# Kernel tuning notes

Measured on AMD Instinct MI355X. Metric: run time of the kernel, lower is better.

## Reference

```python
import jax, jax.numpy as jnp
import numpy as np

B = 512       # batch/feature rows
N = 131072    # node dimension (last axis of x)
E = 131072    # edges per tree level
L = 4         # number of tree levels


def setup_inputs() -> dict:
    key = jax.random.key(0)
    kx, k0, k1, k2, k3 = jax.random.split(key, 5)
    x = jax.random.normal(kx, (B, N), dtype=jnp.float32)
    edges0 = jax.random.randint(k0, (2, E), 0, N, dtype=jnp.int64)
    edges1 = jax.random.randint(k1, (2, E), 0, N, dtype=jnp.int64)
    edges2 = jax.random.randint(k2, (2, E), 0, N, dtype=jnp.int64)
    edges3 = jax.random.randint(k3, (2, E), 0, N, dtype=jnp.int64)
    return {"x": x, "edges0": edges0, "edges1": edges1,
            "edges2": edges2, "edges3": edges3}


def reference(x, edges0, edges1, edges2, edges3):
    # TreeAggregation.forward: iterate levels from deepest (last) to root
    # (first). Per level: gather x at src along last dim, scatter-add into
    # dst (duplicate dst indices accumulate, matching torch.index_add).
    for edges in (edges3, edges2, edges1, edges0):
        src = edges[0, :]
        dst = edges[1, :]
        values = x[:, src]                 # [B, E] gather
        x = x.at[:, dst].add(values)       # scatter-add with duplicates
    return x
```

## Files before the change

### kernel.cpp

```cpp
#include <hip/hip_runtime.h>
#include <hip/hip_bf16.h>

#define BATCH 512
#define NNODE 131072
#define NEDGE 131072
#define NLAYER 4
#define SCAN_BLK 1024
#define SCAN_NBLK (NNODE / SCAN_BLK)
#define PCAP (8 * NEDGE)

__device__ int g_counts[NLAYER][NNODE];
__device__ int g_offs[NLAYER][NNODE];
__device__ int g_cursor[NLAYER][NNODE];
__device__ int g_srcl[NLAYER][NEDGE];
__device__ int g_bsums[NLAYER][SCAN_NBLK];

__device__ int p_cnt[2][NNODE];
__device__ int p_offs[2][NNODE];
__device__ int p_srcl[2][PCAP];
__device__ int p_bsums[2][SCAN_NBLK];

typedef unsigned int uivec4 __attribute__((ext_vector_type(4)));
typedef float fvec4 __attribute__((ext_vector_type(4)));

__device__ __forceinline__ void nt_store_u4(uint4* p, uint4 v) {
    uivec4 w = {v.x, v.y, v.z, v.w};
    __builtin_nontemporal_store(w, reinterpret_cast<uivec4*>(p));
}

__device__ __forceinline__ void nt_store_f4(float* p, float4 v) {
    fvec4 w = {v.x, v.y, v.z, v.w};
    __builtin_nontemporal_store(w, reinterpret_cast<fvec4*>(p));
}

__global__ void zero_counts_k() {
    int i = blockIdx.x * blockDim.x + threadIdx.x;
    ((int*)g_counts)[i] = 0;
}

__global__ void hist_k(const int* __restrict__ p0, const int* __restrict__ p1,
                       const int* __restrict__ p2, const int* __restrict__ p3) {
    int i = blockIdx.x * blockDim.x + threadIdx.x;
    int layer = i >> 17;
    int e = i & (NEDGE - 1);
    const int* eg = layer == 0 ? p0 : layer == 1 ? p1 : layer == 2 ? p2 : p3;
    atomicAdd(&g_counts[layer][eg[NEDGE + e]], 1);
}

__global__ void scan_block_k() {
    __shared__ int sh[SCAN_BLK];
    int layer = blockIdx.x / SCAN_NBLK;
    int blk = blockIdx.x % SCAN_NBLK;
    int t = threadIdx.x;
    int i = blk * SCAN_BLK + t;
    int own = g_counts[layer][i];
    sh[t] = own;
    __syncthreads();
    for (int off = 1; off < SCAN_BLK; off <<= 1) {
        int v = (t >= off) ? sh[t - off] : 0;
        __syncthreads();
        sh[t] += v;
        __syncthreads();
    }
    g_offs[layer][i] = sh[t] - own;
    if (t == SCAN_BLK - 1) g_bsums[layer][blk] = sh[t];
}

__global__ void scan_bsums_k() {
    __shared__ int sh[SCAN_NBLK];
    int layer = blockIdx.x;
    int t = threadIdx.x;
    int own = g_bsums[layer][t];
    sh[t] = own;
    __syncthreads();
    for (int off = 1; off < SCAN_NBLK; off <<= 1) {
        int v = (t >= off) ? sh[t - off] : 0;
        __syncthreads();
        sh[t] += v;
        __syncthreads();
    }
    g_bsums[layer][t] = sh[t] - own;
}

__global__ void scan_add_k() {
    int layer = blockIdx.x / SCAN_NBLK;
    int blk = blockIdx.x % SCAN_NBLK;
    int i = blk * SCAN_BLK + threadIdx.x;
    int o = g_offs[layer][i] + g_bsums[layer][blk];
    g_offs[layer][i] = o;
    g_cursor[layer][i] = o;
}

__global__ void fill_k(const int* __restrict__ p0, const int* __restrict__ p1,
                       const int* __restrict__ p2, const int* __restrict__ p3) {
    int i = blockIdx.x * blockDim.x + threadIdx.x;
    int layer = i >> 17;
    int e = i & (NEDGE - 1);
    const int* eg = layer == 0 ? p0 : layer == 1 ? p1 : layer == 2 ? p2 : p3;
    int s = eg[e];
    int d = eg[NEDGE + e];
    int p = atomicAdd(&g_cursor[layer][d], 1);
    g_srcl[layer][p] = s;
}

__global__ void count_pair_k() {
    int i = blockIdx.x * blockDim.x + threadIdx.x;
    int pr = i >> 17;
    int d = i & (NNODE - 1);
    int U = pr * 2, V = pr * 2 + 1;
    int c = 1 + g_counts[U][d];
    int vb = g_offs[V][d], vd = g_counts[V][d];
    for (int j = 0; j < vd; ++j) {
        int s = g_srcl[V][vb + j];
        c += 1 + g_counts[U][s];
    }
    p_cnt[pr][d] = c;
}

__global__ void pscan_block_k() {
    __shared__ int sh[SCAN_BLK];
    int pr = blockIdx.x / SCAN_NBLK;
    int blk = blockIdx.x % SCAN_NBLK;
    int t = threadIdx.x;
    int i = blk * SCAN_BLK + t;
    int own = p_cnt[pr][i];
    sh[t] = own;
    __syncthreads();
    for (int off = 1; off < SCAN_BLK; off <<= 1) {
        int v = (t >= off) ? sh[t - off] : 0;
        __syncthreads();
        sh[t] += v;
        __syncthreads();
    }
    p_offs[pr][i] = sh[t] - own;
    if (t == SCAN_BLK - 1) p_bsums[pr][blk] = sh[t];
}

__global__ void pscan_bsums_k() {
    __shared__ int sh[SCAN_NBLK];
    int pr = blockIdx.x;
    int t = threadIdx.x;
    int own = p_bsums[pr][t];
    sh[t] = own;
    __syncthreads();
    for (int off = 1; off < SCAN_NBLK; off <<= 1) {
        int v = (t >= off) ? sh[t - off] : 0;
        __syncthreads();
        sh[t] += v;
        __syncthreads();
    }
    p_bsums[pr][t] = sh[t] - own;
}

__global__ void pscan_add_k() {
    int pr = blockIdx.x / SCAN_NBLK;
    int blk = blockIdx.x % SCAN_NBLK;
    int i = blk * SCAN_BLK + threadIdx.x;
    p_offs[pr][i] += p_bsums[pr][blk];
}

__global__ void fill_pair_k() {
    int i = blockIdx.x * blockDim.x + threadIdx.x;
    int pr = i >> 17;
    int d = i & (NNODE - 1);
    int U = pr * 2, V = pr * 2 + 1;
    int p = p_offs[pr][d];
    int* buf = p_srcl[pr];
    buf[p++] = d;
    int ub = g_offs[U][d], ud = g_counts[U][d];
    for (int j = 0; j < ud; ++j) buf[p++] = g_srcl[U][ub + j];
    int vb = g_offs[V][d], vd = g_counts[V][d];
    for (int j = 0; j < vd; ++j) {
        int s = g_srcl[V][vb + j];
        buf[p++] = s;
        int sb = g_offs[U][s], sd = g_counts[U][s];
        for (int k = 0; k < sd; ++k) buf[p++] = g_srcl[U][sb + k];
    }
}

__global__ void transpose_bf_k(const float* __restrict__ in, unsigned short* __restrict__ out) {
    __shared__ float tile[64][65];
    int c0 = blockIdx.x * 64;
    int r0 = blockIdx.y * 64;
    int tx = threadIdx.x;
    int ty = threadIdx.y;
    float4 v[4];
#pragma unroll
    for (int i = 0; i < 4; ++i)
        v[i] = *reinterpret_cast<const float4*>(&in[(size_t)(r0 + ty + 16 * i) * NNODE + c0 + 4 * tx]);
#pragma unroll
    for (int i = 0; i < 4; ++i) {
        tile[ty + 16 * i][4 * tx + 0] = v[i].x;
        tile[ty + 16 * i][4 * tx + 1] = v[i].y;
        tile[ty + 16 * i][4 * tx + 2] = v[i].z;
        tile[ty + 16 * i][4 * tx + 3] = v[i].w;
    }
    __syncthreads();
#pragma unroll
    for (int i = 0; i < 4; ++i) {
        int n = c0 + ty + 16 * i;
        ushort4 w;
        __hip_bfloat16 h0 = __float2bfloat16(tile[4 * tx + 0][ty + 16 * i]);
        __hip_bfloat16 h1 = __float2bfloat16(tile[4 * tx + 1][ty + 16 * i]);
        __hip_bfloat16 h2 = __float2bfloat16(tile[4 * tx + 2][ty + 16 * i]);
        __hip_bfloat16 h3 = __float2bfloat16(tile[4 * tx + 3][ty + 16 * i]);
        w.x = *reinterpret_cast<unsigned short*>(&h0);
        w.y = *reinterpret_cast<unsigned short*>(&h1);
        w.z = *reinterpret_cast<unsigned short*>(&h2);
        w.w = *reinterpret_cast<unsigned short*>(&h3);
        *reinterpret_cast<ushort4*>(&out[(size_t)n * BATCH + r0 + 4 * tx]) = w;
    }
}

__device__ __forceinline__ void gacc8(float* a, uint4 v) {
    a[0] += __uint_as_float(v.x << 16);
    a[1] += __uint_as_float(v.x & 0xffff0000u);
    a[2] += __uint_as_float(v.y << 16);
    a[3] += __uint_as_float(v.y & 0xffff0000u);
    a[4] += __uint_as_float(v.z << 16);
    a[5] += __uint_as_float(v.z & 0xffff0000u);
    a[6] += __uint_as_float(v.w << 16);
    a[7] += __uint_as_float(v.w & 0xffff0000u);
}

__device__ __forceinline__ unsigned pack2(float lo, float hi) {
    __hip_bfloat16 l = __float2bfloat16(lo);
    __hip_bfloat16 h = __float2bfloat16(hi);
    return (unsigned)*reinterpret_cast<unsigned short*>(&l) |
           ((unsigned)*reinterpret_cast<unsigned short*>(&h) << 16);
}

__device__ __forceinline__ void gather_body_bf(const uint4* __restrict__ cur,
                                               const int* __restrict__ sl, int deg, int q,
                                               float acc[8]) {
    float A[8] = {0, 0, 0, 0, 0, 0, 0, 0};
    float B_[8] = {0, 0, 0, 0, 0, 0, 0, 0};
    float C_[8] = {0, 0, 0, 0, 0, 0, 0, 0};
    float D_[8] = {0, 0, 0, 0, 0, 0, 0, 0};
    int j = 0;
    for (; j + 4 <= deg; j += 4) {
        uint4 v0 = cur[(size_t)sl[j + 0] * 64 + q];
        uint4 v1 = cur[(size_t)sl[j + 1] * 64 + q];
        uint4 v2 = cur[(size_t)sl[j + 2] * 64 + q];
        uint4 v3 = cur[(size_t)sl[j + 3] * 64 + q];
        gacc8(A, v0);
        gacc8(B_, v1);
        gacc8(C_, v2);
        gacc8(D_, v3);
    }
    for (; j < deg; ++j) {
        uint4 v = cur[(size_t)sl[j] * 64 + q];
        gacc8(A, v);
    }
#pragma unroll
    for (int k = 0; k < 8; ++k) acc[k] = A[k] + B_[k] + C_[k] + D_[k];
}

__global__ void gather_p_k(const uint4* __restrict__ cur, uint4* __restrict__ out,
                           int pr) {
    int t = threadIdx.x;
    int n = blockIdx.x * 8 + (t >> 6);
    int q = t & 63;
    int beg = p_offs[pr][n];
    int deg = p_cnt[pr][n];
    float acc[8];
    gather_body_bf(cur, &p_srcl[pr][beg], deg, q, acc);
    uint4 w;
    w.x = pack2(acc[0], acc[1]);
    w.y = pack2(acc[2], acc[3]);
    w.z = pack2(acc[4], acc[5]);
    w.w = pack2(acc[6], acc[7]);
    nt_store_u4(&out[(size_t)n * 64 + q], w);
}

__global__ void __launch_bounds__(1024) gather_tr_p_k(const uint4* __restrict__ cur,
                                                      float* __restrict__ out, int pr) {
    __shared__ float lds[16][520];
    int t = threadIdx.x;
    int n0 = blockIdx.x * 16;
    int nn = t >> 6;
    int q = t & 63;
    int n = n0 + nn;
    int beg = p_offs[pr][n];
    int deg = p_cnt[pr][n];
    float acc[8];
    gather_body_bf(cur, &p_srcl[pr][beg], deg, q, acc);
    float4* lrow = reinterpret_cast<float4*>(&lds[nn][8 * q]);
    lrow[0] = make_float4(acc[0], acc[1], acc[2], acc[3]);
    lrow[1] = make_float4(acc[4], acc[5], acc[6], acc[7]);
    __syncthreads();
    int c = t & 3;
    int rb = t >> 2;
#pragma unroll
    for (int iter = 0; iter < 2; ++iter) {
        int b = iter * 256 + rb;
        float4 w;
        w.x = lds[4 * c + 0][b];
        w.y = lds[4 * c + 1][b];
        w.z = lds[4 * c + 2][b];
        w.w = lds[4 * c + 3][b];
        nt_store_f4(&out[(size_t)b * NNODE + n0 + 4 * c], w);
    }
}

extern "C" void kernel_launch(void* const* d_in, const int* in_sizes, int n_in,
                              void* d_out, int out_size, void* d_ws, size_t ws_size,
                              hipStream_t stream) {
    const float* x = (const float*)d_in[0];
    const int* p0 = (const int*)d_in[4];
    const int* p1 = (const int*)d_in[3];
    const int* p2 = (const int*)d_in[2];
    const int* p3 = (const int*)d_in[1];

    unsigned short* WS0 = (unsigned short*)d_ws;
    unsigned short* WS1 = WS0 + (size_t)NNODE * BATCH;
    float* OUT = (float*)d_out;

    zero_counts_k<<<NLAYER * NNODE / 1024, 1024, 0, stream>>>();
    hist_k<<<NLAYER * NEDGE / 1024, 1024, 0, stream>>>(p0, p1, p2, p3);
    scan_block_k<<<NLAYER * SCAN_NBLK, SCAN_BLK, 0, stream>>>();
    scan_bsums_k<<<NLAYER, SCAN_NBLK, 0, stream>>>();
    scan_add_k<<<NLAYER * SCAN_NBLK, SCAN_BLK, 0, stream>>>();
    fill_k<<<NLAYER * NEDGE / 1024, 1024, 0, stream>>>(p0, p1, p2, p3);

    count_pair_k<<<2 * NNODE / 1024, 1024, 0, stream>>>();
    pscan_block_k<<<2 * SCAN_NBLK, SCAN_BLK, 0, stream>>>();
    pscan_bsums_k<<<2, SCAN_NBLK, 0, stream>>>();
    pscan_add_k<<<2 * SCAN_NBLK, SCAN_BLK, 0, stream>>>();
    fill_pair_k<<<2 * NNODE / 256, 256, 0, stream>>>();

    transpose_bf_k<<<dim3(NNODE / 64, BATCH / 64), dim3(16, 16), 0, stream>>>(x, WS0);

    gather_p_k<<<NNODE / 8, 512, 0, stream>>>((const uint4*)WS0, (uint4*)WS1, 0);
    gather_tr_p_k<<<NNODE / 16, 1024, 0, stream>>>((const uint4*)WS1, OUT, 1);
}
```

Measured before the change: 506.1 us.

## Split batch dimension into two halves for gather kernels to improve cache locality

```diff
diff --git a/kernel.cpp b/kernel.cpp
--- a/kernel.cpp
+++ b/kernel.cpp
@@ -20,12 +20,12 @@
 __device__ int p_srcl[2][PCAP];
 __device__ int p_bsums[2][SCAN_NBLK];
 
-typedef unsigned int uivec4 __attribute__((ext_vector_type(4)));
+typedef unsigned int uivec2 __attribute__((ext_vector_type(2)));
 typedef float fvec4 __attribute__((ext_vector_type(4)));
 
-__device__ __forceinline__ void nt_store_u4(uint4* p, uint4 v) {
-    uivec4 w = {v.x, v.y, v.z, v.w};
-    __builtin_nontemporal_store(w, reinterpret_cast<uivec4*>(p));
+__device__ __forceinline__ void nt_store_u2(uint2* p, uint2 v) {
+    uivec2 w = {v.x, v.y};
+    __builtin_nontemporal_store(w, reinterpret_cast<uivec2*>(p));
 }
 
 __device__ __forceinline__ void nt_store_f4(float* p, float4 v) {
@@ -212,15 +212,11 @@
     }
 }
 
-__device__ __forceinline__ void gacc8(float* a, uint4 v) {
+__device__ __forceinline__ void gacc4(float* a, uint2 v) {
     a[0] += __uint_as_float(v.x << 16);
     a[1] += __uint_as_float(v.x & 0xffff0000u);
     a[2] += __uint_as_float(v.y << 16);
     a[3] += __uint_as_float(v.y & 0xffff0000u);
-    a[4] += __uint_as_float(v.z << 16);
-    a[5] += __uint_as_float(v.z & 0xffff0000u);
-    a[6] += __uint_as_float(v.w << 16);
-    a[7] += __uint_as_float(v.w & 0xffff0000u);
 }
 
 __device__ __forceinline__ unsigned pack2(float lo, float hi) {
@@ -230,77 +226,73 @@
            ((unsigned)*reinterpret_cast<unsigned short*>(&h) << 16);
 }
 
-__device__ __forceinline__ void gather_body_bf(const uint4* __restrict__ cur,
-                                               const int* __restrict__ sl, int deg, int q,
-                                               float acc[8]) {
-    float A[8] = {0, 0, 0, 0, 0, 0, 0, 0};
-    float B_[8] = {0, 0, 0, 0, 0, 0, 0, 0};
-    float C_[8] = {0, 0, 0, 0, 0, 0, 0, 0};
-    float D_[8] = {0, 0, 0, 0, 0, 0, 0, 0};
+__device__ __forceinline__ void gather_body_bf2(const uint2* __restrict__ cur,
+                                                const int* __restrict__ sl, int deg, int idx,
+                                                float acc[4]) {
+    float A[4] = {0, 0, 0, 0};
+    float B_[4] = {0, 0, 0, 0};
+    float C_[4] = {0, 0, 0, 0};
+    float D_[4] = {0, 0, 0, 0};
     int j = 0;
     for (; j + 4 <= deg; j += 4) {
-        uint4 v0 = cur[(size_t)sl[j + 0] * 64 + q];
-        uint4 v1 = cur[(size_t)sl[j + 1] * 64 + q];
-        uint4 v2 = cur[(size_t)sl[j + 2] * 64 + q];
-        uint4 v3 = cur[(size_t)sl[j + 3] * 64 + q];
-        gacc8(A, v0);
-        gacc8(B_, v1);
-        gacc8(C_, v2);
-        gacc8(D_, v3);
+        uint2 v0 = cur[(size_t)sl[j + 0] * 128 + idx];
+        uint2 v1 = cur[(size_t)sl[j + 1] * 128 + idx];
+        uint2 v2 = cur[(size_t)sl[j + 2] * 128 + idx];
+        uint2 v3 = cur[(size_t)sl[j + 3] * 128 + idx];
+        gacc4(A, v0);
+        gacc4(B_, v1);
+        gacc4(C_, v2);
+        gacc4(D_, v3);
     }
     for (; j < deg; ++j) {
-        uint4 v = cur[(size_t)sl[j] * 64 + q];
-        gacc8(A, v);
+        uint2 v = cur[(size_t)sl[j] * 128 + idx];
+        gacc4(A, v);
     }
 #pragma unroll
-    for (int k = 0; k < 8; ++k) acc[k] = A[k] + B_[k] + C_[k] + D_[k];
-}
-
-__global__ void gather_p_k(const uint4* __restrict__ cur, uint4* __restrict__ out,
-                           int pr) {
+    for (int k = 0; k < 4; ++k) acc[k] = A[k] + B_[k] + C_[k] + D_[k];
+}
+
+__global__ void gather_p_k(const uint2* __restrict__ cur, uint2* __restrict__ out,
+                           int pr, int h) {
     int t = threadIdx.x;
     int n = blockIdx.x * 8 + (t >> 6);
     int q = t & 63;
+    int idx = h * 64 + q;
     int beg = p_offs[pr][n];
     int deg = p_cnt[pr][n];
-    float acc[8];
-    gather_body_bf(cur, &p_srcl[pr][beg], deg, q, acc);
-    uint4 w;
+    float acc[4];
+    gather_body_bf2(cur, &p_srcl[pr][beg], deg, idx, acc);
+    uint2 w;
     w.x = pack2(acc[0], acc[1]);
     w.y = pack2(acc[2], acc[3]);
-    w.z = pack2(acc[4], acc[5]);
-    w.w = pack2(acc[6], acc[7]);
-    nt_store_u4(&out[(size_t)n * 64 + q], w);
-}
-
-__global__ void __launch_bounds__(1024) gather_tr_p_k(const uint4* __restrict__ cur,
-                                                      float* __restrict__ out, int pr) {
-    __shared__ float lds[16][520];
+    nt_store_u2(&out[(size_t)n * 128 + idx], w);
+}
+
+__global__ void __launch_bounds__(1024) gather_tr_p_k(const uint2* __restrict__ cur,
+                                                      float* __restrict__ out, int pr, int h) {
+    __shared__ float lds[16][260];
     int t = threadIdx.x;
     int n0 = blockIdx.x * 16;
     int nn = t >> 6;
     int q = t & 63;
+    int idx = h * 64 + q;
     int n = n0 + nn;
     int beg = p_offs[pr][n];
     int deg = p_cnt[pr][n];
-    float acc[8];
-    gather_body_bf(cur, &p_srcl[pr][beg], deg, q, acc);
-    float4* lrow = reinterpret_cast<float4*>(&lds[nn][8 * q]);
+    float acc[4];
+    gather_body_bf2(cur, &p_srcl[pr][beg], deg, idx, acc);
+    float4* lrow = reinterpret_cast<float4*>(&lds[nn][4 * q]);
     lrow[0] = make_float4(acc[0], acc[1], acc[2], acc[3]);
-    lrow[1] = make_float4(acc[4], acc[5], acc[6], acc[7]);
     __syncthreads();
     int c = t & 3;
     int rb = t >> 2;
-#pragma unroll
-    for (int iter = 0; iter < 2; ++iter) {
-        int b = iter * 256 + rb;
-        float4 w;
-        w.x = lds[4 * c + 0][b];
-        w.y = lds[4 * c + 1][b];
-        w.z = lds[4 * c + 2][b];
-        w.w = lds[4 * c + 3][b];
-        nt_store_f4(&out[(size_t)b * NNODE + n0 + 4 * c], w);
-    }
+    int b = h * 256 + rb;
+    float4 w;
+    w.x = lds[4 * c + 0][rb];
+    w.y = lds[4 * c + 1][rb];
+    w.z = lds[4 * c + 2][rb];
+    w.w = lds[4 * c + 3][rb];
+    nt_store_f4(&out[(size_t)b * NNODE + n0 + 4 * c], w);
 }
 
 extern "C" void kernel_launch(void* const* d_in, const int* in_sizes, int n_in,
@@ -331,6 +323,8 @@
 
     transpose_bf_k<<<dim3(NNODE / 64, BATCH / 64), dim3(16, 16), 0, stream>>>(x, WS0);
 
-    gather_p_k<<<NNODE / 8, 512, 0, stream>>>((const uint4*)WS0, (uint4*)WS1, 0);
-    gather_tr_p_k<<<NNODE / 16, 1024, 0, stream>>>((const uint4*)WS1, OUT, 1);
-}
+    gather_p_k<<<NNODE / 8, 512, 0, stream>>>((const uint2*)WS0, (uint2*)WS1, 0, 0);
+    gather_p_k<<<NNODE / 8, 512, 0, stream>>>((const uint2*)WS0, (uint2*)WS1, 0, 1);
+    gather_tr_p_k<<<NNODE / 16, 1024, 0, stream>>>((const uint2*)WS1, OUT, 1, 0);
+    gather_tr_p_k<<<NNODE / 16, 1024, 0, stream>>>((const uint2*)WS1, OUT, 1, 1);
+}
```

New measurement: 513.1 us. Within noise of the previous version (+1.4%).

## Sort nodes by degree and gather four nodes per wave with separate transpose

Applied to the files above, without the earlier changes.

```diff
diff --git a/kernel.cpp b/kernel.cpp
--- a/kernel.cpp
+++ b/kernel.cpp
@@ -19,6 +19,9 @@
 __device__ int p_offs[2][NNODE];
 __device__ int p_srcl[2][PCAP];
 __device__ int p_bsums[2][SCAN_NBLK];
+
+__device__ int s_hist[2][64], s_cur[2][64];
+__device__ int d_perm[2][NNODE];
 
 typedef unsigned int uivec4 __attribute__((ext_vector_type(4)));
 typedef float fvec4 __attribute__((ext_vector_type(4)));
@@ -178,6 +181,56 @@
     }
 }
 
+__global__ void sort_zero_k() {
+    int t = threadIdx.x;
+    ((int*)s_hist)[t] = 0;
+}
+
+__global__ void histp_k() {
+    __shared__ int lh[64];
+    int t = threadIdx.x;
+    int pr = blockIdx.x >> 7;
+    int n = (blockIdx.x & 127) * 1024 + t;
+    if (t < 64) lh[t] = 0;
+    __syncthreads();
+    int b = 63 - min(p_cnt[pr][n], 63);
+    atomicAdd(&lh[b], 1);
+    __syncthreads();
+    if (t < 64) atomicAdd(&s_hist[pr][t], lh[t]);
+}
+
+__global__ void sort_scan_k() {
+    __shared__ int sh[2][64];
+    int t = threadIdx.x;
+    int pr = t >> 6;
+    int k = t & 63;
+    sh[pr][k] = s_hist[pr][k];
+    __syncthreads();
+    for (int off = 1; off < 64; off <<= 1) {
+        int v = (k >= off) ? sh[pr][k - off] : 0;
+        __syncthreads();
+        sh[pr][k] += v;
+        __syncthreads();
+    }
+    s_cur[pr][k] = sh[pr][k] - s_hist[pr][k];
+}
+
+__global__ void permp_k() {
+    __shared__ int lh[64];
+    __shared__ int lbase[64];
+    int t = threadIdx.x;
+    int pr = blockIdx.x >> 7;
+    int n = (blockIdx.x & 127) * 1024 + t;
+    if (t < 64) lh[t] = 0;
+    __syncthreads();
+    int b = 63 - min(p_cnt[pr][n], 63);
+    int lpos = atomicAdd(&lh[b], 1);
+    __syncthreads();
+    if (t < 64) lbase[t] = lh[t] ? atomicAdd(&s_cur[pr][t], lh[t]) : 0;
+    __syncthreads();
+    d_perm[pr][lbase[b] + lpos] = n;
+}
+
 __global__ void transpose_bf_k(const float* __restrict__ in, unsigned short* __restrict__ out) {
     __shared__ float tile[64][65];
     int c0 = blockIdx.x * 64;
@@ -212,6 +265,34 @@
     }
 }
 
+__global__ void transpose_fb_k(const unsigned short* __restrict__ in, float* __restrict__ out) {
+    __shared__ float tile[64][65];
+    int n0 = blockIdx.x * 64;
+    int b0 = blockIdx.y * 64;
+    int tx = threadIdx.x;
+    int ty = threadIdx.y;
+#pragma unroll
+    for (int i = 0; i < 4; ++i) {
+        int nl = ty + 16 * i;
+        ushort4 w = *reinterpret_cast<const ushort4*>(&in[(size_t)(n0 + nl) * BATCH + b0 + 4 * tx]);
+        tile[nl][4 * tx + 0] = __uint_as_float((unsigned)w.x << 16);
+        tile[nl][4 * tx + 1] = __uint_as_float((unsigned)w.y << 16);
+        tile[nl][4 * tx + 2] = __uint_as_float((unsigned)w.z << 16);
+        tile[nl][4 * tx + 3] = __uint_as_float((unsigned)w.w << 16);
+    }
+    __syncthreads();
+#pragma unroll
+    for (int i = 0; i < 4; ++i) {
+        int bl = ty + 16 * i;
+        float4 w;
+        w.x = tile[4 * tx + 0][bl];
+        w.y = tile[4 * tx + 1][bl];
+        w.z = tile[4 * tx + 2][bl];
+        w.w = tile[4 * tx + 3][bl];
+        nt_store_f4(&out[(size_t)(b0 + bl) * NNODE + n0 + 4 * tx], w);
+    }
+}
+
 __device__ __forceinline__ void gacc8(float* a, uint4 v) {
     a[0] += __uint_as_float(v.x << 16);
     a[1] += __uint_as_float(v.x & 0xffff0000u);
@@ -230,76 +311,57 @@
            ((unsigned)*reinterpret_cast<unsigned short*>(&h) << 16);
 }
 
-__device__ __forceinline__ void gather_body_bf(const uint4* __restrict__ cur,
-                                               const int* __restrict__ sl, int deg, int q,
-                                               float acc[8]) {
-    float A[8] = {0, 0, 0, 0, 0, 0, 0, 0};
-    float B_[8] = {0, 0, 0, 0, 0, 0, 0, 0};
-    float C_[8] = {0, 0, 0, 0, 0, 0, 0, 0};
-    float D_[8] = {0, 0, 0, 0, 0, 0, 0, 0};
+__global__ void __launch_bounds__(512) gather4_k(const uint4* __restrict__ cur,
+                                                 uint4* __restrict__ out, int pr) {
+    int t = threadIdx.x;
+    int q = t & 63;
+    int wv = t >> 6;
+    int base = blockIdx.x * 32 + wv * 4;
+    int n[4], deg[4];
+    const int* sl[4];
+#pragma unroll
+    for (int k = 0; k < 4; ++k) {
+        n[k] = d_perm[pr][base + k];
+        deg[k] = __builtin_amdgcn_readfirstlane(p_cnt[pr][n[k]]);
+        sl[k] = &p_srcl[pr][p_offs[pr][n[k]]];
+    }
+    float acc[4][8];
+#pragma unroll
+    for (int k = 0; k < 4; ++k)
+#pragma unroll
+        for (int m = 0; m < 8; ++m) acc[k][m] = 0.f;
+    int jmax = max(max(deg[0], deg[1]), max(deg[2], deg[3]));
     int j = 0;
-    for (; j + 4 <= deg; j += 4) {
-        uint4 v0 = cur[(size_t)sl[j + 0] * 64 + q];
-        uint4 v1 = cur[(size_t)sl[j + 1] * 64 + q];
-        uint4 v2 = cur[(size_t)sl[j + 2] * 64 + q];
-        uint4 v3 = cur[(size_t)sl[j + 3] * 64 + q];
-        gacc8(A, v0);
-        gacc8(B_, v1);
-        gacc8(C_, v2);
-        gacc8(D_, v3);
-    }
-    for (; j < deg; ++j) {
-        uint4 v = cur[(size_t)sl[j] * 64 + q];
-        gacc8(A, v);
-    }
-#pragma unroll
-    for (int k = 0; k < 8; ++k) acc[k] = A[k] + B_[k] + C_[k] + D_[k];
-}
-
-__global__ void gather_p_k(const uint4* __restrict__ cur, uint4* __restrict__ out,
-                           int pr) {
-    int t = threadIdx.x;
-    int n = blockIdx.x * 8 + (t >> 6);
-    int q = t & 63;
-    int beg = p_offs[pr][n];
-    int deg = p_cnt[pr][n];
-    float acc[8];
-    gather_body_bf(cur, &p_srcl[pr][beg], deg, q, acc);
-    uint4 w;
-    w.x = pack2(acc[0], acc[1]);
-    w.y = pack2(acc[2], acc[3]);
-    w.z = pack2(acc[4], acc[5]);
-    w.w = pack2(acc[6], acc[7]);
-    nt_store_u4(&out[(size_t)n * 64 + q], w);
-}
-
-__global__ void __launch_bounds__(1024) gather_tr_p_k(const uint4* __restrict__ cur,
-                                                      float* __restrict__ out, int pr) {
-    __shared__ float lds[16][520];
-    int t = threadIdx.x;
-    int n0 = blockIdx.x * 16;
-    int nn = t >> 6;
-    int q = t & 63;
-    int n = n0 + nn;
-    int beg = p_offs[pr][n];
-    int deg = p_cnt[pr][n];
-    float acc[8];
-    gather_body_bf(cur, &p_srcl[pr][beg], deg, q, acc);
-    float4* lrow = reinterpret_cast<float4*>(&lds[nn][8 * q]);
-    lrow[0] = make_float4(acc[0], acc[1], acc[2], acc[3]);
-    lrow[1] = make_float4(acc[4], acc[5], acc[6], acc[7]);
-    __syncthreads();
-    int c = t & 3;
-    int rb = t >> 2;
-#pragma unroll
-    for (int iter = 0; iter < 2; ++iter) {
-        int b = iter * 256 + rb;
-        float4 w;
-        w.x = lds[4 * c + 0][b];
-        w.y = lds[4 * c + 1][b];
-        w.z = lds[4 * c + 2][b];
-        w.w = lds[4 * c + 3][b];
-        nt_store_f4(&out[(size_t)b * NNODE + n0 + 4 * c], w);
+    for (; j + 2 <= jmax; j += 2) {
+        uint4 v[8];
+#pragma unroll
+        for (int k = 0; k < 4; ++k) {
+            if (j < deg[k])     v[2 * k]     = cur[(size_t)sl[k][j] * 64 + q];
+            if (j + 1 < deg[k]) v[2 * k + 1] = cur[(size_t)sl[k][j + 1] * 64 + q];
+        }
+#pragma unroll
+        for (int k = 0; k < 4; ++k) {
+            if (j < deg[k])     gacc8(acc[k], v[2 * k]);
+            if (j + 1 < deg[k]) gacc8(acc[k], v[2 * k + 1]);
+        }
+    }
+    if (j < jmax) {
+        uint4 v[4];
+#pragma unroll
+        for (int k = 0; k < 4; ++k)
+            if (j < deg[k]) v[k] = cur[(size_t)sl[k][j] * 64 + q];
+#pragma unroll
+        for (int k = 0; k < 4; ++k)
+            if (j < deg[k]) gacc8(acc[k], v[k]);
+    }
+#pragma unroll
+    for (int k = 0; k < 4; ++k) {
+        uint4 w;
+        w.x = pack2(acc[k][0], acc[k][1]);
+        w.y = pack2(acc[k][2], acc[k][3]);
+        w.z = pack2(acc[k][4], acc[k][5]);
+        w.w = pack2(acc[k][6], acc[k][7]);
+        nt_store_u4(&out[(size_t)n[k] * 64 + q], w);
     }
 }
 
@@ -329,8 +391,14 @@
     pscan_add_k<<<2 * SCAN_NBLK, SCAN_BLK, 0, stream>>>();
     fill_pair_k<<<2 * NNODE / 256, 256, 0, stream>>>();
 
+    sort_zero_k<<<1, 128, 0, stream>>>();
+    histp_k<<<2 * NNODE / 1024, 1024, 0, stream>>>();
+    sort_scan_k<<<1, 128, 0, stream>>>();
+    permp_k<<<2 * NNODE / 1024, 1024, 0, stream>>>();
+
     transpose_bf_k<<<dim3(NNODE / 64, BATCH / 64), dim3(16, 16), 0, stream>>>(x, WS0);
 
-    gather_p_k<<<NNODE / 8, 512, 0, stream>>>((const uint4*)WS0, (uint4*)WS1, 0);
-    gather_tr_p_k<<<NNODE / 16, 1024, 0, stream>>>((const uint4*)WS1, OUT, 1);
-}
+    gather4_k<<<NNODE / 32, 512, 0, stream>>>((const uint4*)WS0, (uint4*)WS1, 0);
+    gather4_k<<<NNODE / 32, 512, 0, stream>>>((const uint4*)WS1, (uint4*)WS0, 1);
+    transpose_fb_k<<<dim3(NNODE / 64, BATCH / 64), dim3(16, 16), 0, stream>>>(WS0, OUT);
+}
```

Measured after the change: 488.6 us. -3.5%, faster.
